# Performance work log

Hardware: AMD Instinct MI355X
Metric: run time of the kernel (lower is better)

The kernel has to match this reference:

```python
import jax, jax.numpy as jnp
import numpy as np

N_NODES, N_EDGES, B, L = 20000, 320000, 64, 48
EMB, OUT, HEADS, HID = 256, 64, 4, 512
S_DIM, R_DIM = 64, 64
TIME_NUM, CAT_NUM = 48, 201


def lrelu(x, s=0.2):
    return jnp.where(x >= 0, x, s * x)


def gru_cell(x, h, Wi, Wh, bi, bh):
    # PyTorch GRUCell math
    gi = x @ Wi.T + bi
    gh = h @ Wh.T + bh
    ir, iz, ig = jnp.split(gi, 3, axis=-1)
    hr, hz, hg = jnp.split(gh, 3, axis=-1)
    r = jax.nn.sigmoid(ir + hr)
    z = jax.nn.sigmoid(iz + hz)
    n = jnp.tanh(ig + r * hg)
    return (1.0 - z) * n + z * h


def gru_seq(x, Wi, Wh, bi, bh, reverse=False):
    # x: [B,L,D] -> [B,L,H]
    xs = jnp.swapaxes(x, 0, 1)
    if reverse:
        xs = xs[::-1]
    h0 = jnp.zeros((x.shape[0], Wh.shape[1]), x.dtype)

    def step(h, xt):
        h2 = gru_cell(xt, h, Wi, Wh, bi, bh)
        return h2, h2

    _, ys = jax.lax.scan(step, h0, xs)
    if reverse:
        ys = ys[::-1]
    return jnp.swapaxes(ys, 0, 1)


def setup_inputs() -> dict:
    key = jax.random.key(0)
    ks = iter(jax.random.split(key, 64))
    f32 = jnp.float32

    def rn(shape, s=0.1):
        return (s * jax.random.normal(next(ks), shape)).astype(f32)

    inp = {
        'graph_x': jnp.arange(N_NODES),
        'edge_index': jax.random.randint(next(ks), (2, N_EDGES), 0, N_NODES),
        'edge_attr': jax.random.uniform(next(ks), (N_EDGES,), f32),
        'batch_x': jax.random.randint(next(ks), (B, L), 0, N_NODES),
        'batch_time': jax.random.randint(next(ks), (B, L), 0, TIME_NUM),
        'batch_cat': jax.random.randint(next(ks), (B, L), 0, CAT_NUM),
        'poi_time': jax.random.randint(next(ks), (N_NODES,), 0, TIME_NUM),
        'poi_cat': jax.random.randint(next(ks), (N_NODES,), 0, CAT_NUM),
        # params
        'node_emb': rn((N_NODES, EMB), 1.0),
        'W_gat': rn((EMB, HEADS * OUT), 0.05),
        'att_src': rn((HEADS, OUT), 0.05),
        'att_dst': rn((HEADS, OUT), 0.05),
        'gat_bias': rn((HEADS * OUT,)),
        'time_table': rn((TIME_NUM, EMB), 1.0),
        'cat_table': rn((CAT_NUM, EMB), 1.0),
        'W_w': rn((EMB, 3 * EMB)), 'b_w': rn((EMB,)),
        'Wi_f': rn((3 * HID, EMB), 0.05), 'Wh_f': rn((3 * HID, HID), 0.05),
        'bi_f': jnp.zeros((3 * HID,), f32), 'bh_f': jnp.zeros((3 * HID,), f32),
        'Wi_bw': rn((3 * HID, EMB), 0.05), 'Wh_bw': rn((3 * HID, HID), 0.05),
        'bi_bw': jnp.zeros((3 * HID,), f32), 'bh_bw': jnp.zeros((3 * HID,), f32),
        'Wi_u': rn((3 * HID, 2 * HID), 0.05), 'Wh_u': rn((3 * HID, HID), 0.05),
        'bi_u': jnp.zeros((3 * HID,), f32), 'bh_u': jnp.zeros((3 * HID,), f32),
        'Ws_m': rn((S_DIM, 2 * HID)), 'bs_m': rn((S_DIM,)),
        'Ws_lv': rn((S_DIM, 2 * HID)), 'bs_lv': rn((S_DIM,)),
        'Wr_m': rn((R_DIM, HID)), 'br_m': rn((R_DIM,)),
        'Wr_lv': rn((R_DIM, HID)), 'br_lv': rn((R_DIM,)),
        'Wp1_i': rn((3 * HID, R_DIM), 0.05), 'Wp1_h': rn((3 * HID, HID), 0.05),
        'bp1_i': jnp.zeros((3 * HID,), f32), 'bp1_h': jnp.zeros((3 * HID,), f32),
        'Wp2_i': rn((3 * HID, HID), 0.05), 'Wp2_h': rn((3 * HID, HID), 0.05),
        'bp2_i': jnp.zeros((3 * HID,), f32), 'bp2_h': jnp.zeros((3 * HID,), f32),
        'Wpm': rn((R_DIM, HID)), 'bpm': rn((R_DIM,)),
        'Wplv': rn((R_DIM, HID)), 'bplv': rn((R_DIM,)),
        'Wd': rn((N_NODES, S_DIM + R_DIM)), 'bd': rn((N_NODES,)),
    }
    return inp


def forward(graph_x, edge_index, edge_attr, batch_x, batch_time, batch_cat,
            poi_time, poi_cat, node_emb, W_gat, att_src, att_dst, gat_bias,
            time_table, cat_table, W_w, b_w, Wi_f, Wh_f, bi_f, bh_f,
            Wi_bw, Wh_bw, bi_bw, bh_bw, Wi_u, Wh_u, bi_u, bh_u,
            Ws_m, bs_m, Ws_lv, bs_lv, Wr_m, br_m, Wr_lv, br_lv,
            Wp1_i, Wp1_h, bp1_i, bp1_h, Wp2_i, Wp2_h, bp2_i, bp2_h,
            Wpm, bpm, Wplv, bplv, Wd, bd):
    Bn, Ln = batch_x.shape
    N = node_emb.shape[0]
    heads, C = att_src.shape

    # --- weighted GAT layer over the POI graph ---
    h = node_emb[graph_x]                                   # [N, EMB]
    xW = (h @ W_gat).reshape(N, heads, C)                   # [N, H, C]
    src, dst = edge_index[0], edge_index[1]
    e = lrelu((xW * att_src).sum(-1)[src] + (xW * att_dst).sum(-1)[dst])  # [E, H]
    emax = jax.ops.segment_max(e, dst, num_segments=N)
    a = jnp.exp(e - emax[dst])
    asum = jax.ops.segment_sum(a, dst, num_segments=N)
    att = a / (asum[dst] + 1e-16)
    msg = (att * edge_attr[:, None])[:, :, None] * xW[src]  # [E, H, C]
    p = jax.ops.segment_sum(msg, dst, num_segments=N).reshape(N, heads * C) + gat_bias

    # --- per-step feature build ---
    p_h = p[batch_x]                                        # [B, L, EMB]
    t_e = time_table[batch_time]
    c_e = cat_table[batch_cat]
    ph = jnp.concatenate([p_h, t_e, c_e], axis=2) @ W_w.T + b_w  # [B, L, EMB]

    # --- posterior encode: biGRU -> s, uniGRU -> r ---
    f_fwd = gru_seq(ph, Wi_f, Wh_f, bi_f, bh_f)
    f_bwd = gru_seq(ph, Wi_bw, Wh_bw, bi_bw, bh_bw, reverse=True)
    features = jnp.concatenate([f_fwd, f_bwd], axis=2)      # [B, L, 2H]
    Hh = Wh_f.shape[1]
    frontal = features[:, Ln - 1, :Hh]
    backward = features[:, 0, Hh:2 * Hh]
    g = jnp.concatenate([frontal, backward], axis=1)
    s_mean = lrelu(g @ Ws_m.T + bs_m)
    s_logvar = lrelu(g @ Ws_lv.T + bs_lv)

    key = jax.random.key(42)
    k1, k2, k3 = jax.random.split(key, 3)
    s_post = s_mean + jax.random.normal(k1, s_mean.shape, s_mean.dtype) * jnp.exp(0.5 * s_logvar)

    r_feat = gru_seq(features, Wi_u, Wh_u, bi_u, bh_u)      # [B, L, H]
    r_mean = r_feat @ Wr_m.T + br_m
    r_logvar = r_feat @ Wr_lv.T + br_lv
    r_post = r_mean + jax.random.normal(k2, r_mean.shape, r_mean.dtype) * jnp.exp(0.5 * r_logvar)

    # --- prior: 2-layer GRUCell unroll fed with shifted r_post ---
    Rd = r_post.shape[2]
    r_in = jnp.concatenate([jnp.zeros((Bn, 1, Rd), r_post.dtype), r_post[:, :-1]], axis=1)
    r_in_t = jnp.swapaxes(r_in, 0, 1)                       # [L, B, R]
    eps = jax.random.normal(k3, (Ln, Bn, Rd), r_post.dtype)

    def pstep(carry, xe):
        h1, h2 = carry
        rt, ep = xe
        h1 = gru_cell(rt, h1, Wp1_i, Wp1_h, bp1_i, bp1_h)
        h2 = gru_cell(h1, h2, Wp2_i, Wp2_h, bp2_i, bp2_h)
        mt = h2 @ Wpm.T + bpm
        lvt = h2 @ Wplv.T + bplv
        rp = mt + ep * jnp.exp(0.5 * lvt)
        return (h1, h2), (mt, lvt, rp)

    h10 = jnp.zeros((Bn, Hh), r_post.dtype)
    h20 = jnp.zeros((Bn, Hh), r_post.dtype)
    _, (ms, lvs, rps) = jax.lax.scan(pstep, (h10, h20), (r_in_t, eps))
    r_mean_prior = jnp.swapaxes(ms, 0, 1)
    r_logvar_prior = jnp.swapaxes(lvs, 0, 1)
    r_prior = jnp.swapaxes(rps, 0, 1)

    # --- decode ---
    s_expand = jnp.broadcast_to(s_post[:, None, :], (Bn, Ln, s_post.shape[1]))
    zf = jnp.concatenate([r_post, s_expand], axis=2)
    recon_x = zf @ Wd.T + bd                                # [B, L, node_num]
    return (s_mean, s_logvar, s_post, r_mean, r_logvar, r_post,
            r_mean_prior, r_logvar_prior, r_prior, recon_x)


def reference(graph_x, edge_index, edge_attr, batch_x, batch_time, batch_cat,
              poi_time, poi_cat, node_emb, W_gat, att_src, att_dst, gat_bias,
              time_table, cat_table, W_w, b_w, Wi_f, Wh_f, bi_f, bh_f,
              Wi_bw, Wh_bw, bi_bw, bh_bw, Wi_u, Wh_u, bi_u, bh_u,
              Ws_m, bs_m, Ws_lv, bs_lv, Wr_m, br_m, Wr_lv, br_lv,
              Wp1_i, Wp1_h, bp1_i, bp1_h, Wp2_i, Wp2_h, bp2_i, bp2_h,
              Wpm, bpm, Wplv, bplv, Wd, bd):
    return forward(graph_x, edge_index, edge_attr, batch_x, batch_time, batch_cat,
                   poi_time, poi_cat, node_emb, W_gat, att_src, att_dst, gat_bias,
                   time_table, cat_table, W_w, b_w, Wi_f, Wh_f, bi_f, bh_f,
                   Wi_bw, Wh_bw, bi_bw, bh_bw, Wi_u, Wh_u, bi_u, bh_u,
                   Ws_m, bs_m, Ws_lv, bs_lv, Wr_m, br_m, Wr_lv, br_lv,
                   Wp1_i, Wp1_h, bp1_i, bp1_h, Wp2_i, Wp2_h, bp2_i, bp2_h,
                   Wpm, bpm, Wplv, bplv, Wd, bd)
```

## Files before the change

kernel.cpp:

```cpp
#include <hip/hip_runtime.h>
#include <stdint.h>
#include <stddef.h>

#define DEV __device__ __forceinline__

typedef float f32x4 __attribute__((ext_vector_type(4)));

__host__ __device__ inline void tf2x32(uint32_t k0, uint32_t k1,
                                       uint32_t x0, uint32_t x1,
                                       uint32_t* o0, uint32_t* o1) {
  uint32_t ks2 = k0 ^ k1 ^ 0x1BD11BDAu;
  uint32_t ks[3] = {k0, k1, ks2};
  x0 += k0; x1 += k1;
  const uint32_t R[8] = {13u,15u,26u,6u,17u,29u,16u,24u};
  for (int r = 0; r < 5; ++r) {
    const uint32_t* rot = (r & 1) ? (R + 4) : R;
    for (int i = 0; i < 4; ++i) {
      x0 += x1;
      uint32_t d = rot[i];
      x1 = (x1 << d) | (x1 >> (32u - d));
      x1 ^= x0;
    }
    x0 += ks[(r + 1) % 3];
    x1 += ks[(r + 2) % 3] + (uint32_t)(r + 1);
  }
  *o0 = x0; *o1 = x1;
}

DEV float erfinv_approx(float x) {
  float w = -logf((1.0f - x) * (1.0f + x));
  float p;
  if (w < 5.0f) {
    w = w - 2.5f;
    p = 2.81022636e-08f;
    p = fmaf(p, w, 3.43273939e-07f);
    p = fmaf(p, w, -3.5233877e-06f);
    p = fmaf(p, w, -4.39150654e-06f);
    p = fmaf(p, w, 0.00021858087f);
    p = fmaf(p, w, -0.00125372503f);
    p = fmaf(p, w, -0.00417768164f);
    p = fmaf(p, w, 0.246640727f);
    p = fmaf(p, w, 1.50140941f);
  } else {
    w = sqrtf(w) - 3.0f;
    p = -0.000200214257f;
    p = fmaf(p, w, 0.000100950558f);
    p = fmaf(p, w, 0.00134934322f);
    p = fmaf(p, w, -0.00367342844f);
    p = fmaf(p, w, 0.00573950773f);
    p = fmaf(p, w, -0.0076224613f);
    p = fmaf(p, w, 0.00943887047f);
    p = fmaf(p, w, 1.00167406f);
    p = fmaf(p, w, 2.83297682f);
  }
  return p * x;
}

DEV float normal_part(uint32_t ka, uint32_t kb, uint32_t idx) {
  uint32_t b1, b2;
  tf2x32(ka, kb, 0u, idx, &b1, &b2);
  uint32_t bits = b1 ^ b2;
  float f = __uint_as_float((bits >> 9) | 0x3f800000u) - 1.0f;
  const float lo = -0.99999994f;
  float u = f * 2.0f + lo;
  u = fmaxf(lo, u);
  return 1.41421356f * erfinv_approx(u);
}

DEV float lrelu(float x) { return x >= 0.f ? x : 0.2f * x; }
DEV float sigm(float x) { return 1.0f / (1.0f + expf(-x)); }

DEV float gru_out(float ir, float iz, float ig, float hr, float hz, float hg, float hprev) {
  float r = sigm(ir + hr);
  float z = sigm(iz + hz);
  float n = tanhf(ig + r * hg);
  return (1.0f - z) * n + z * hprev;
}

DEV float dot4f(float4 a, float4 b, float acc) {
  return fmaf(a.x, b.x, fmaf(a.y, b.y, fmaf(a.z, b.z, fmaf(a.w, b.w, acc))));
}

template <int K4>
DEV void dot2(const float* __restrict__ h, const float* __restrict__ w0,
              const float* __restrict__ w1, float& a0, float& a1) {
  const float4* h4 = (const float4*)h;
  const float4* p0 = (const float4*)w0;
  const float4* p1 = (const float4*)w1;
  #pragma unroll 4
  for (int k = 0; k < K4; ++k) {
    float4 hv = h4[k];
    float4 v0 = p0[k], v1 = p1[k];
    a0 = dot4f(hv, v0, a0);
    a1 = dot4f(hv, v1, a1);
  }
}

template <int K4>
DEV void dotT3p(const float* __restrict__ hp, int b,
                const float* __restrict__ w0, const float* __restrict__ w1,
                const float* __restrict__ w2, float& a0, float& a1, float& a2) {
  const float4* __restrict__ w04 = (const float4*)w0;
  const float4* __restrict__ w14 = (const float4*)w1;
  const float4* __restrict__ w24 = (const float4*)w2;
  const float4* __restrict__ h4 = (const float4*)hp;
  #pragma unroll
  for (int k4 = 0; k4 < K4; ++k4) {
    float4 hv = h4[k4 * 64 + b];
    a0 = dot4f(w04[k4], hv, a0);
    a1 = dot4f(w14[k4], hv, a1);
    a2 = dot4f(w24[k4], hv, a2);
  }
}

template <int K4>
DEV void dotT3_lds(const float* __restrict__ hl, int b,
                   const float* __restrict__ w0, const float* __restrict__ w1,
                   const float* __restrict__ w2, float& a0, float& a1, float& a2) {
  const float4* __restrict__ h4 = (const float4*)hl;
  const float4* __restrict__ w04 = (const float4*)w0;
  const float4* __restrict__ w14 = (const float4*)w1;
  const float4* __restrict__ w24 = (const float4*)w2;
  #pragma unroll 8
  for (int k4 = 0; k4 < K4; ++k4) {
    float4 hv = h4[k4 * 64 + b];
    a0 = dot4f(w04[k4], hv, a0);
    a1 = dot4f(w14[k4], hv, a1);
    a2 = dot4f(w24[k4], hv, a2);
  }
}

template <int N16>
DEV void stage_lds(float* __restrict__ dst, const float* __restrict__ src) {
  const float4* __restrict__ s4 = (const float4*)src;
  float4* __restrict__ d4 = (float4*)dst;
  int tid = threadIdx.x;
  constexpr int CH = (N16 < 16) ? N16 : 16;
  #pragma unroll
  for (int r = 0; r < N16; r += CH) {
    float4 v[CH];
    #pragma unroll
    for (int u = 0; u < CH; ++u) v[u] = s4[(size_t)(r + u) * 256 + tid];
    #pragma unroll
    for (int u = 0; u < CH; ++u) d4[(size_t)(r + u) * 256 + tid] = v[u];
  }
}

DEV size_t pk(int k, int b) { return (size_t)(k >> 2) * 256 + b * 4 + (k & 3); }

DEV void coh_store_i(int* p, int v) {
  asm volatile("global_store_dword %0, %1, off sc0 sc1" :: "v"(p), "v"(v) : "memory");
}
DEV void coh_store_f(float* p, float v) {
  asm volatile("global_store_dword %0, %1, off sc0 sc1" :: "v"(p), "v"(v) : "memory");
}
DEV void coh_store_f4(float* p, f32x4 v) {
  asm volatile("global_store_dwordx4 %0, %1, off sc0 sc1" :: "v"(p), "v"(v) : "memory");
}
DEV int coh_load_i(const int* p) {
  int v;
  asm volatile("global_load_dword %0, %1, off sc0 sc1\n\ts_waitcnt vmcnt(0)"
               : "=v"(v) : "v"(p) : "memory");
  return v;
}

DEV void flag_barrier(int* __restrict__ flags, int nblk, int myidx, int gen) {
  asm volatile("s_waitcnt vmcnt(0)" ::: "memory");
  __syncthreads();
  if (threadIdx.x == 0) coh_store_i(flags + myidx, gen);
  if ((int)threadIdx.x < nblk) {
    int spins = 0;
    while (coh_load_i(flags + threadIdx.x) < gen) {
      __builtin_amdgcn_s_sleep(16);
      if (++spins > (1 << 19)) break;
    }
  }
  __syncthreads();
}

DEV void wait_group(const int* __restrict__ flags, int nblk, int thr) {
  if ((int)threadIdx.x < nblk) {
    int spins = 0;
    while (coh_load_i(flags + threadIdx.x) < thr) {
      __builtin_amdgcn_s_sleep(16);
      if (++spins > (1 << 19)) break;
    }
  }
  __syncthreads();
}

DEV void store_packed_tile4(float* dst_t, const float (*smem)[64], int j0) {
  if (threadIdx.x < 64) {
    int bb = threadIdx.x;
    f32x4 v;
    v.x = smem[0][bb];
    v.y = smem[1][bb];
    v.z = smem[2][bb];
    v.w = smem[3][bb];
    coh_store_f4(dst_t + (size_t)(j0 >> 2) * 256 + bb * 4, v);
  }
}

#define GBM 128
#define GBN 128
#define GBK 16

__global__ __launch_bounds__(256) void gemm_nt(
    const float* __restrict__ A, const float* __restrict__ Bt,
    const float* __restrict__ bias, float* __restrict__ C,
    int M, int N, int K, const int* __restrict__ gatherA, int trGI) {
  __shared__ float As[GBK][GBM + 4];
  __shared__ float Bs[GBK][GBN + 4];
  const int bm = blockIdx.y * GBM;
  const int bn = blockIdx.x * GBN;
  const int tid = threadIdx.x;
  const int tx = tid & 15;
  const int ty = tid >> 4;
  float acc[8][8];
  #pragma unroll
  for (int i = 0; i < 8; ++i)
    #pragma unroll
    for (int j = 0; j < 8; ++j) acc[i][j] = 0.f;

  for (int k0 = 0; k0 < K; k0 += GBK) {
    #pragma unroll
    for (int s = 0; s < 2; ++s) {
      int f = tid + s * 256;
      int r = f >> 2, kq = f & 3;
      int row = bm + r;
      float4 v = make_float4(0.f, 0.f, 0.f, 0.f);
      if (row < M) {
        int ar = gatherA ? gatherA[row] : row;
        v = *(const float4*)&A[(size_t)ar * K + k0 + kq * 4];
      }
      As[kq * 4 + 0][r] = v.x;
      As[kq * 4 + 1][r] = v.y;
      As[kq * 4 + 2][r] = v.z;
      As[kq * 4 + 3][r] = v.w;
    }
    #pragma unroll
    for (int s = 0; s < 2; ++s) {
      int f = tid + s * 256;
      int r = f >> 2, kq = f & 3;
      int col = bn + r;
      float4 v = make_float4(0.f, 0.f, 0.f, 0.f);
      if (col < N) v = *(const float4*)&Bt[(size_t)col * K + k0 + kq * 4];
      Bs[kq * 4 + 0][r] = v.x;
      Bs[kq * 4 + 1][r] = v.y;
      Bs[kq * 4 + 2][r] = v.z;
      Bs[kq * 4 + 3][r] = v.w;
    }
    __syncthreads();
    #pragma unroll
    for (int kk = 0; kk < GBK; ++kk) {
      float4 a0 = *(const float4*)&As[kk][ty * 4];
      float4 a1 = *(const float4*)&As[kk][64 + ty * 4];
      float4 b0 = *(const float4*)&Bs[kk][tx * 4];
      float4 b1 = *(const float4*)&Bs[kk][64 + tx * 4];
      float av[8] = {a0.x, a0.y, a0.z, a0.w, a1.x, a1.y, a1.z, a1.w};
      float bv[8] = {b0.x, b0.y, b0.z, b0.w, b1.x, b1.y, b1.z, b1.w};
      #pragma unroll
      for (int i = 0; i < 8; ++i)
        #pragma unroll
        for (int j = 0; j < 8; ++j)
          acc[i][j] = fmaf(av[i], bv[j], acc[i][j]);
    }
    __syncthreads();
  }
  #pragma unroll
  for (int i = 0; i < 8; ++i) {
    int row = bm + ((i < 4) ? (ty * 4 + i) : (64 + ty * 4 + i - 4));
    if (row >= M) continue;
    if (trGI) {
      #pragma unroll
      for (int j = 0; j < 8; ++j) {
        int col = bn + ((j < 4) ? (tx * 4 + j) : (64 + tx * 4 + j - 4));
        if (col >= N) continue;
        float v = acc[i][j] + (bias ? bias[col] : 0.f);
        int bb = row / 48, tt = row - bb * 48;
        C[((size_t)tt * N + col) * 64 + bb] = v;
      }
    } else {
      #pragma unroll
      for (int g = 0; g < 2; ++g) {
        int col0 = bn + g * 64 + tx * 4;
        if (col0 + 3 >= N) continue;
        float4 v;
        v.x = acc[i][g * 4 + 0] + (bias ? bias[col0 + 0] : 0.f);
        v.y = acc[i][g * 4 + 1] + (bias ? bias[col0 + 1] : 0.f);
        v.z = acc[i][g * 4 + 2] + (bias ? bias[col0 + 2] : 0.f);
        v.w = acc[i][g * 4 + 3] + (bias ? bias[col0 + 3] : 0.f);
        *(float4*)&C[(size_t)row * N + col0] = v;
      }
    }
  }
}

__global__ void k_transpose(const float* __restrict__ W, float* __restrict__ Wt,
                            int rows, int cols) {
  int idx = blockIdx.x * 256 + threadIdx.x;
  if (idx >= rows * cols) return;
  int r = idx / cols, c = idx % cols;
  Wt[(size_t)c * rows + r] = W[idx];
}

__global__ void k_count_deg(const int* __restrict__ dst, int* __restrict__ deg, int nE) {
  int e = blockIdx.x * 256 + threadIdx.x;
  if (e < nE) atomicAdd(&deg[dst[e]], 1);
}

__global__ __launch_bounds__(1024) void k_scan(const int* __restrict__ deg,
                                               int* __restrict__ off,
                                               int* __restrict__ cursor, int n) {
  __shared__ int tmp[1024];
  __shared__ int carry_s;
  if (threadIdx.x == 0) carry_s = 0;
  __syncthreads();
  for (int base = 0; base < n; base += 1024) {
    int i = base + (int)threadIdx.x;
    int v = (i < n) ? deg[i] : 0;
    tmp[threadIdx.x] = v;
    __syncthreads();
    for (int s = 1; s < 1024; s <<= 1) {
      int t = (threadIdx.x >= (unsigned)s) ? tmp[threadIdx.x - s] : 0;
      __syncthreads();
      tmp[threadIdx.x] += t;
      __syncthreads();
    }
    int incl = tmp[threadIdx.x];
    int base_c = carry_s;
    int excl = incl - v;
    if (i < n) { off[i] = base_c + excl; cursor[i] = base_c + excl; }
    __syncthreads();
    if (threadIdx.x == 1023) carry_s = base_c + incl;
    __syncthreads();
  }
  if (threadIdx.x == 0) off[n] = carry_s;
}

__global__ void k_scatter(const int* __restrict__ dst, int* __restrict__ cursor,
                          int* __restrict__ csr, int nE) {
  int e = blockIdx.x * 256 + threadIdx.x;
  if (e < nE) {
    int pos = atomicAdd(&cursor[dst[e]], 1);
    csr[pos] = e;
  }
}

__global__ void k_alpha(const float* __restrict__ xW, const float* __restrict__ att_src,
                        const float* __restrict__ att_dst, float* __restrict__ as_,
                        float* __restrict__ ad_) {
  int i = blockIdx.x * 256 + threadIdx.x;
  if (i >= 80000) return;
  int n = i >> 2, h = i & 3;
  const float* xr = xW + (size_t)n * 256 + h * 64;
  const float* s = att_src + h * 64;
  const float* d = att_dst + h * 64;
  float a = 0.f, b = 0.f;
  dot2<16>(xr, s, d, a, b);
  as_[i] = a;
  ad_[i] = b;
}

__global__ __launch_bounds__(256) void k_gat_node(
    const float* __restrict__ xW, const float* __restrict__ as_,
    const float* __restrict__ ad_, const int* __restrict__ off,
    const int* __restrict__ csr, const int* __restrict__ esrc,
    const float* __restrict__ eattr, const float* __restrict__ gat_bias,
    float* __restrict__ p) {
  int n = blockIdx.x;
  int h = threadIdx.x >> 6;
  int c = threadIdx.x & 63;
  int s0 = off[n], s1 = off[n + 1];
  float adn = ad_[n * 4 + h];
  float m = -3.0e38f;
  for (int idx = s0; idx < s1; ++idx) {
    int e = csr[idx];
    int s = esrc[e];
    float ev = lrelu(as_[s * 4 + h] + adn);
    m = fmaxf(m, ev);
  }
  float sum = 0.f;
  for (int idx = s0; idx < s1; ++idx) {
    int e = csr[idx];
    int s = esrc[e];
    float ev = lrelu(as_[s * 4 + h] + adn);
    sum += expf(ev - m);
  }
  float acc = 0.f;
  for (int idx = s0; idx < s1; ++idx) {
    int e = csr[idx];
    int s = esrc[e];
    float ev = lrelu(as_[s * 4 + h] + adn);
    float w = expf(ev - m) / (sum + 1e-16f) * eattr[e];
    acc = fmaf(w, xW[(size_t)s * 256 + h * 64 + c], acc);
  }
  p[(size_t)n * 256 + h * 64 + c] = acc + gat_bias[h * 64 + c];
}

__global__ void k_build_X(const float* __restrict__ p, const float* __restrict__ tt,
                          const float* __restrict__ ct, const int* __restrict__ bx,
                          const int* __restrict__ btm, const int* __restrict__ bct,
                          float* __restrict__ X) {
  int idx = blockIdx.x * 256 + threadIdx.x;
  if (idx >= 3072 * 768) return;
  int rl = idx / 768, c = idx % 768;
  float v;
  if (c < 256) v = p[(size_t)bx[rl] * 256 + c];
  else if (c < 512) v = tt[(size_t)btm[rl] * 256 + (c - 256)];
  else v = ct[(size_t)bct[rl] * 256 + (c - 512)];
  X[idx] = v;
}

__global__ __launch_bounds__(256, 1) void k_gru_bidir_fused(
    const float* __restrict__ giT_f, const float* __restrict__ giT_b,
    const float* __restrict__ Wh_f, const float* __restrict__ bh_f,
    const float* __restrict__ Wh_b, const float* __restrict__ bh_b,
    float* __restrict__ features, float* __restrict__ hTb,
    int* __restrict__ flags) {
  __shared__ float lds_h[32768];
  __shared__ float smem[4][64];
  int w = threadIdx.x >> 6;
  int b = threadIdx.x & 63;
  int slot = blockIdx.x * 4 + w;
  int dir = slot >> 9;
  int j = slot & 511;
  int j0 = (blockIdx.x * 4) & 511;
  int gbid = blockIdx.x & 127;
  int* gflags = flags + dir * 128;
  const float* Wh = dir ? Wh_b : Wh_f;
  const float* bh = dir ? bh_b : bh_f;
  const float* gi = dir ? giT_b : giT_f;
  const float* w0 = Wh + (size_t)j * 512;
  const float* w1 = Wh + (size_t)(512 + j) * 512;
  const float* w2 = Wh + (size_t)(1024 + j) * 512;
  float bhr = bh[j], bhz = bh[512 + j], bhg = bh[1024 + j];
  float* hD = hTb + (size_t)dir * 48 * 32768;
  for (int s = 0; s < 48; ++s) {
    int t = dir ? (47 - s) : s;
    const float* gir = gi + (size_t)t * 98304;
    float giv0 = gir[j * 64 + b];
    float giv1 = gir[(512 + j) * 64 + b];
    float giv2 = gir[(1024 + j) * 64 + b];
    float hr = bhr, hz = bhz, hg = bhg, hprev = 0.f;
    if (s > 0) {
      int tp = dir ? (t + 1) : (t - 1);
      stage_lds<32>(lds_h, hD + (size_t)tp * 32768);
      __syncthreads();
      dotT3_lds<128>(lds_h, b, w0, w1, w2, hr, hz, hg);
      hprev = lds_h[pk(j, b)];
    }
    float hnew = gru_out(giv0, giv1, giv2, hr, hz, hg, hprev);
    smem[w][b] = hnew;
    features[((size_t)(b * 48 + t)) * 1024 + dir * 512 + j] = hnew;
    __syncthreads();
    store_packed_tile4(hD + (size_t)t * 32768, smem, j0);
    flag_barrier(gflags, 128, gbid, s + 1);
  }
}

__global__ __launch_bounds__(256, 1) void k_gru_u_fused(
    const float* __restrict__ giT, const float* __restrict__ Wh,
    const float* __restrict__ bh, float* __restrict__ r_feat,
    float* __restrict__ hU, int* __restrict__ flags) {
  __shared__ float lds_h[32768];
  __shared__ float smem[4][64];
  int w = threadIdx.x >> 6;
  int b = threadIdx.x & 63;
  int j = blockIdx.x * 4 + w;
  int j0 = blockIdx.x * 4;
  const float* w0 = Wh + (size_t)j * 512;
  const float* w1 = Wh + (size_t)(512 + j) * 512;
  const float* w2 = Wh + (size_t)(1024 + j) * 512;
  float bhr = bh[j], bhz = bh[512 + j], bhg = bh[1024 + j];
  for (int s = 0; s < 48; ++s) {
    const float* gir = giT + (size_t)s * 98304;
    float giv0 = gir[j * 64 + b];
    float giv1 = gir[(512 + j) * 64 + b];
    float giv2 = gir[(1024 + j) * 64 + b];
    float hr = bhr, hz = bhz, hg = bhg, hprev = 0.f;
    if (s > 0) {
      stage_lds<32>(lds_h, hU + (size_t)(s - 1) * 32768);
      __syncthreads();
      dotT3_lds<128>(lds_h, b, w0, w1, w2, hr, hz, hg);
      hprev = lds_h[pk(j, b)];
    }
    float hnew = gru_out(giv0, giv1, giv2, hr, hz, hg, hprev);
    smem[w][b] = hnew;
    r_feat[((size_t)(b * 48 + s)) * 512 + j] = hnew;
    __syncthreads();
    store_packed_tile4(hU + (size_t)s * 32768, smem, j0);
    flag_barrier(flags, 128, blockIdx.x, s + 1);
  }
}

__global__ __launch_bounds__(256, 1) void k_prior_fused(
    const float* __restrict__ r_post,
    const float* __restrict__ Wp1_i, const float* __restrict__ Wp1_h,
    const float* __restrict__ bp1_i, const float* __restrict__ bp1_h,
    const float* __restrict__ Wp2_i, const float* __restrict__ Wp2_h,
    const float* __restrict__ bp2_i, const float* __restrict__ bp2_h,
    float* __restrict__ h1S, float* __restrict__ h2S,
    float* __restrict__ rT, int* __restrict__ flags) {
  __shared__ float lds_h[32768];
  __shared__ float smem[4][64];
  int w = threadIdx.x >> 6;
  int b = threadIdx.x & 63;
  int cell = blockIdx.x >> 7;
  int gbid = blockIdx.x & 127;
  int slot = blockIdx.x * 4 + w;
  int j = slot & 511;
  int j0 = (blockIdx.x * 4) & 511;
  int* flagsA = flags;
  int* flagsB = flags + 128;

  if (cell == 0) {
    int tid = gbid * 256 + threadIdx.x;
    for (int x = tid; x < 48 * 64 * 64; x += 32768) {
      int b0 = x & 63;
      int i0 = (x >> 6) & 63;
      int t0 = x >> 12;
      coh_store_f(rT + (size_t)t0 * 4096 + pk(i0, b0),
                  r_post[((size_t)(b0 * 48 + t0)) * 64 + i0]);
    }
    flag_barrier(flagsA, 128, gbid, 1);

    const float* wi0 = Wp1_i + (size_t)j * 64;
    const float* wi1 = Wp1_i + (size_t)(512 + j) * 64;
    const float* wi2 = Wp1_i + (size_t)(1024 + j) * 64;
    const float* wh0 = Wp1_h + (size_t)j * 512;
    const float* wh1 = Wp1_h + (size_t)(512 + j) * 512;
    const float* wh2 = Wp1_h + (size_t)(1024 + j) * 512;
    float bir = bp1_i[j], biz = bp1_i[512 + j], big = bp1_i[1024 + j];
    float bhr = bp1_h[j], bhz = bp1_h[512 + j], bhg = bp1_h[1024 + j];
    for (int k = 0; k < 48; ++k) {
      float ir = bir, iz = biz, ig = big;
      float hr = bhr, hz = bhz, hg = bhg, hprev = 0.f;
      if (k > 0) {
        stage_lds<32>(lds_h, h1S + (size_t)(k - 1) * 32768);
        dotT3p<16>(rT + (size_t)(k - 1) * 4096, b, wi0, wi1, wi2, ir, iz, ig);
        __syncthreads();
        dotT3_lds<128>(lds_h, b, wh0, wh1, wh2, hr, hz, hg);
        hprev = lds_h[pk(j, b)];
      }
      smem[w][b] = gru_out(ir, iz, ig, hr, hz, hg, hprev);
      __syncthreads();
      store_packed_tile4(h1S + (size_t)k * 32768, smem, j0);
      flag_barrier(flagsA, 128, gbid, k + 2);
    }
  } else {
    const float* wi0 = Wp2_i + (size_t)j * 512;
    const float* wi1 = Wp2_i + (size_t)(512 + j) * 512;
    const float* wi2 = Wp2_i + (size_t)(1024 + j) * 512;
    const float* wh0 = Wp2_h + (size_t)j * 512;
    const float* wh1 = Wp2_h + (size_t)(512 + j) * 512;
    const float* wh2 = Wp2_h + (size_t)(1024 + j) * 512;
    float bir = bp2_i[j], biz = bp2_i[512 + j], big = bp2_i[1024 + j];
    float bhr = bp2_h[j], bhz = bp2_h[512 + j], bhg = bp2_h[1024 + j];
    for (int t = 0; t < 48; ++t) {
      wait_group(flagsA, 128, t + 2);
      stage_lds<32>(lds_h, h1S + (size_t)t * 32768);
      __syncthreads();
      float ir = bir, iz = biz, ig = big;
      dotT3_lds<128>(lds_h, b, wi0, wi1, wi2, ir, iz, ig);
      float hr = bhr, hz = bhz, hg = bhg, hprev = 0.f;
      if (t > 0) {
        __syncthreads();
        stage_lds<32>(lds_h, h2S + (size_t)(t - 1) * 32768);
        __syncthreads();
        dotT3_lds<128>(lds_h, b, wh0, wh1, wh2, hr, hz, hg);
        hprev = lds_h[pk(j, b)];
      }
      smem[w][b] = gru_out(ir, iz, ig, hr, hz, hg, hprev);
      __syncthreads();
      store_packed_tile4(h2S + (size_t)t * 32768, smem, j0);
      flag_barrier(flagsB, 128, gbid, t + 1);
    }
  }
}

__global__ void k_s_head(const float* __restrict__ features,
                         const float* __restrict__ Ws_m, const float* __restrict__ bs_m,
                         const float* __restrict__ Ws_lv, const float* __restrict__ bs_lv,
                         float* __restrict__ out, uint32_t ka, uint32_t kb) {
  int idx = blockIdx.x * 256 + threadIdx.x;
  if (idx >= 4096) return;
  int i = idx & 63, b = idx >> 6;
  const float* fr = features + ((size_t)(b * 48 + 47)) * 1024;
  const float* bk = features + ((size_t)(b * 48 + 0)) * 1024 + 512;
  const float* wm = Ws_m + (size_t)i * 1024;
  const float* wl = Ws_lv + (size_t)i * 1024;
  float m = 0.f, lv = 0.f;
  dot2<128>(fr, wm, wl, m, lv);
  dot2<128>(bk, wm + 512, wl + 512, m, lv);
  m = lrelu(m + bs_m[i]);
  lv = lrelu(lv + bs_lv[i]);
  float nz = normal_part(ka, kb, (uint32_t)idx);
  out[idx] = m;
  out[4096 + idx] = lv;
  out[8192 + idx] = m + nz * expf(0.5f * lv);
}

__global__ void k_r_head(const float* __restrict__ r_feat,
                         const float* __restrict__ Wr_m, const float* __restrict__ br_m,
                         const float* __restrict__ Wr_lv, const float* __restrict__ br_lv,
                         float* __restrict__ out, uint32_t ka, uint32_t kb) {
  int idx = blockIdx.x * 256 + threadIdx.x;
  if (idx >= 196608) return;
  int i = idx & 63;
  int bt = idx >> 6;
  const float* f = r_feat + (size_t)bt * 512;
  float m = 0.f, lv = 0.f;
  dot2<128>(f, Wr_m + (size_t)i * 512, Wr_lv + (size_t)i * 512, m, lv);
  m += br_m[i];
  lv += br_lv[i];
  float nz = normal_part(ka, kb, (uint32_t)idx);
  out[12288 + idx] = m;
  out[208896 + idx] = lv;
  out[405504 + idx] = m + nz * expf(0.5f * lv);
}

__global__ void k_prior_out(const float* __restrict__ h2S,
                            const float* __restrict__ Wpm, const float* __restrict__ bpm,
                            const float* __restrict__ Wplv, const float* __restrict__ bplv,
                            float* __restrict__ out, uint32_t ka, uint32_t kb) {
  int idx = blockIdx.x * 256 + threadIdx.x;
  if (idx >= 196608) return;
  int i = idx & 63;
  int bt = idx >> 6;
  int b = bt & 63;
  int t = bt >> 6;
  const float4* h4 = (const float4*)(h2S + (size_t)t * 32768);
  const float4* wm4 = (const float4*)(Wpm + (size_t)i * 512);
  const float4* wl4 = (const float4*)(Wplv + (size_t)i * 512);
  float m = 0.f, lv = 0.f;
  #pragma unroll 8
  for (int k4 = 0; k4 < 128; ++k4) {
    float4 hv = h4[k4 * 64 + b];
    m = dot4f(wm4[k4], hv, m);
    lv = dot4f(wl4[k4], hv, lv);
  }
  m += bpm[i];
  lv += bplv[i];
  float ep = normal_part(ka, kb, (uint32_t)idx);
  float rp = m + ep * expf(0.5f * lv);
  size_t o = ((size_t)b * 48 + t) * 64 + i;
  out[602112 + o] = m;
  out[798720 + o] = lv;
  out[995328 + o] = rp;
}

__global__ void k_build_zf(const float* __restrict__ out, float* __restrict__ zf) {
  int idx = blockIdx.x * 256 + threadIdx.x;
  if (idx >= 3072 * 128) return;
  int row = idx >> 7, c = idx & 127;
  float v;
  if (c < 64) v = out[405504 + row * 64 + c];
  else v = out[8192 + (row / 48) * 64 + (c - 64)];
  zf[idx] = v;
}

extern "C" void kernel_launch(void* const* d_in, const int* in_sizes, int n_in,
                              void* d_out, int out_size, void* d_ws, size_t ws_size,
                              hipStream_t stream) {
  const int* graph_x = (const int*)d_in[0];
  const int* edge_index = (const int*)d_in[1];
  const float* edge_attr = (const float*)d_in[2];
  const int* batch_x = (const int*)d_in[3];
  const int* batch_time = (const int*)d_in[4];
  const int* batch_cat = (const int*)d_in[5];
  const float* node_emb = (const float*)d_in[8];
  const float* W_gat = (const float*)d_in[9];
  const float* att_src = (const float*)d_in[10];
  const float* att_dst = (const float*)d_in[11];
  const float* gat_bias = (const float*)d_in[12];
  const float* time_table = (const float*)d_in[13];
  const float* cat_table = (const float*)d_in[14];
  const float* W_w = (const float*)d_in[15];
  const float* b_w = (const float*)d_in[16];
  const float* Wi_f = (const float*)d_in[17];
  const float* Wh_f = (const float*)d_in[18];
  const float* bi_f = (const float*)d_in[19];
  const float* bh_f = (const float*)d_in[20];
  const float* Wi_bw = (const float*)d_in[21];
  const float* Wh_bw = (const float*)d_in[22];
  const float* bi_bw = (const float*)d_in[23];
  const float* bh_bw = (const float*)d_in[24];
  const float* Wi_u = (const float*)d_in[25];
  const float* Wh_u = (const float*)d_in[26];
  const float* bi_u = (const float*)d_in[27];
  const float* bh_u = (const float*)d_in[28];
  const float* Ws_m = (const float*)d_in[29];
  const float* bs_m = (const float*)d_in[30];
  const float* Ws_lv = (const float*)d_in[31];
  const float* bs_lv = (const float*)d_in[32];
  const float* Wr_m = (const float*)d_in[33];
  const float* br_m = (const float*)d_in[34];
  const float* Wr_lv = (const float*)d_in[35];
  const float* br_lv = (const float*)d_in[36];
  const float* Wp1_i = (const float*)d_in[37];
  const float* Wp1_h = (const float*)d_in[38];
  const float* bp1_i = (const float*)d_in[39];
  const float* bp1_h = (const float*)d_in[40];
  const float* Wp2_i = (const float*)d_in[41];
  const float* Wp2_h = (const float*)d_in[42];
  const float* bp2_i = (const float*)d_in[43];
  const float* bp2_h = (const float*)d_in[44];
  const float* Wpm = (const float*)d_in[45];
  const float* bpm = (const float*)d_in[46];
  const float* Wplv = (const float*)d_in[47];
  const float* bplv = (const float*)d_in[48];
  const float* Wd = (const float*)d_in[49];
  const float* bd = (const float*)d_in[50];
  float* out = (float*)d_out;

  uint32_t k1a, k1b, k2a, k2b, k3a, k3b;
  tf2x32(0u, 42u, 0u, 0u, &k1a, &k1b);
  tf2x32(0u, 42u, 0u, 1u, &k2a, &k2b);
  tf2x32(0u, 42u, 0u, 2u, &k3a, &k3b);

  float* ws = (float*)d_ws;
  size_t o = 0;
  auto alloc = [&](size_t n) { float* q = ws + o; o += n; return q; };
  float* R1 = alloc(5120000);
  float* R2 = alloc(5120000);
  float* R3 = alloc(4718592);
  float* R4 = alloc(786432);
  float* as_ = alloc(80000);
  float* ad_ = alloc(80000);
  float* Wgt = alloc(65536);
  int* deg = (int*)alloc(20000);
  int* off = (int*)alloc(20001);
  int* cursor = (int*)alloc(20000);
  int* csr = (int*)alloc(320000);
  float* rT = alloc(196608);
  int* flags = (int*)alloc(1024);

  float* xW = R1;
  float* features = R1;
  float* r_feat = R1 + 3145728;
  float* p = R2;
  float* giT_b = R2;
  float* hU = R2;
  float* X = R3;
  float* giT_f = R3;
  float* giT_u = R3;
  float* h1S = R3;
  float* h2S = R3 + 1572864;
  float* ph = R4;
  float* zf = R4;
  float* hTb = out + 1191936;

  const int* esrc = edge_index;
  const int* edst = edge_index + 320000;

  dim3 B(256);

  (void)hipMemsetAsync(deg, 0, 20000 * sizeof(int), stream);
  (void)hipMemsetAsync(flags, 0, 1024 * sizeof(int), stream);

  k_transpose<<<dim3(256), B, 0, stream>>>(W_gat, Wgt, 256, 256);
  k_count_deg<<<dim3(1250), B, 0, stream>>>(edst, deg, 320000);
  k_scan<<<dim3(1), dim3(1024), 0, stream>>>(deg, off, cursor, 20000);
  k_scatter<<<dim3(1250), B, 0, stream>>>(edst, cursor, csr, 320000);
  gemm_nt<<<dim3(2, 157), B, 0, stream>>>(node_emb, Wgt, nullptr, xW,
                                          20000, 256, 256, graph_x, 0);
  k_alpha<<<dim3(313), B, 0, stream>>>(xW, att_src, att_dst, as_, ad_);
  k_gat_node<<<dim3(20000), B, 0, stream>>>(xW, as_, ad_, off, csr, esrc,
                                            edge_attr, gat_bias, p);

  k_build_X<<<dim3(9216), B, 0, stream>>>(p, time_table, cat_table, batch_x,
                                          batch_time, batch_cat, X);
  gemm_nt<<<dim3(2, 24), B, 0, stream>>>(X, W_w, b_w, ph, 3072, 256, 768,
                                         nullptr, 0);

  gemm_nt<<<dim3(12, 24), B, 0, stream>>>(ph, Wi_f, bi_f, giT_f, 3072, 1536, 256,
                                          nullptr, 1);
  gemm_nt<<<dim3(12, 24), B, 0, stream>>>(ph, Wi_bw, bi_bw, giT_b, 3072, 1536, 256,
                                          nullptr, 1);
  k_gru_bidir_fused<<<dim3(256), B, 0, stream>>>(
      giT_f, giT_b, Wh_f, bh_f, Wh_bw, bh_bw, features, hTb, flags);

  k_s_head<<<dim3(16), B, 0, stream>>>(features, Ws_m, bs_m, Ws_lv, bs_lv,
                                       out, k1a, k1b);

  gemm_nt<<<dim3(12, 24), B, 0, stream>>>(features, Wi_u, bi_u, giT_u,
                                          3072, 1536, 1024, nullptr, 1);
  k_gru_u_fused<<<dim3(128), B, 0, stream>>>(giT_u, Wh_u, bh_u, r_feat,
                                             hU, flags + 256);

  k_r_head<<<dim3(768), B, 0, stream>>>(r_feat, Wr_m, br_m, Wr_lv, br_lv,
                                        out, k2a, k2b);

  k_prior_fused<<<dim3(256), B, 0, stream>>>(
      out + 405504, Wp1_i, Wp1_h, bp1_i, bp1_h, Wp2_i, Wp2_h, bp2_i, bp2_h,
      h1S, h2S, rT, flags + 384);
  k_prior_out<<<dim3(768), B, 0, stream>>>(h2S, Wpm, bpm, Wplv, bplv,
                                           out, k3a, k3b);

  k_build_zf<<<dim3(1536), B, 0, stream>>>(out, zf);
  gemm_nt<<<dim3(157, 24), B, 0, stream>>>(zf, Wd, bd, out + 1191936,
                                           3072, 20000, 128, nullptr, 0);
}
```

Measured before the change: 5.106 ms.

## Use 1024-thread blocks in persistent GRU kernels to cut grid barrier participants

The persistent recurrent GRU kernels (bidirectional, u, prior) now run 16 hidden units per block with 1024 threads instead of 4 units with 256 threads. The grid shrinks by 4x, so each per-step flag barrier waits on 32 blocks rather than 128, and each block stages the previous hidden state into LDS once for four times as many output units. Staging and packed-store helpers were rewritten for the wider blocks. In exchange, only 32-64 CUs are used, which lowers aggregate bandwidth for the weight reads done every step.

```diff
diff --git a/kernel.cpp b/kernel.cpp
--- a/kernel.cpp
+++ b/kernel.cpp
@@ -130,20 +130,15 @@
   }
 }
 
-template <int N16>
-DEV void stage_lds(float* __restrict__ dst, const float* __restrict__ src) {
+DEV void stage_lds1k(float* __restrict__ dst, const float* __restrict__ src) {
   const float4* __restrict__ s4 = (const float4*)src;
   float4* __restrict__ d4 = (float4*)dst;
   int tid = threadIdx.x;
-  constexpr int CH = (N16 < 16) ? N16 : 16;
+  float4 v[8];
   #pragma unroll
-  for (int r = 0; r < N16; r += CH) {
-    float4 v[CH];
-    #pragma unroll
-    for (int u = 0; u < CH; ++u) v[u] = s4[(size_t)(r + u) * 256 + tid];
-    #pragma unroll
-    for (int u = 0; u < CH; ++u) d4[(size_t)(r + u) * 256 + tid] = v[u];
-  }
+  for (int u = 0; u < 8; ++u) v[u] = s4[(size_t)u * 1024 + tid];
+  #pragma unroll
+  for (int u = 0; u < 8; ++u) d4[(size_t)u * 1024 + tid] = v[u];
 }
 
 DEV size_t pk(int k, int b) { return (size_t)(k >> 2) * 256 + b * 4 + (k & 3); }
@@ -189,15 +184,16 @@
   __syncthreads();
 }
 
-DEV void store_packed_tile4(float* dst_t, const float (*smem)[64], int j0) {
-  if (threadIdx.x < 64) {
-    int bb = threadIdx.x;
+DEV void store_packed_tile16(float* dst_t, const float (*smem)[64], int j0) {
+  if (threadIdx.x < 256) {
+    int q = threadIdx.x >> 6;
+    int bb = threadIdx.x & 63;
     f32x4 v;
-    v.x = smem[0][bb];
-    v.y = smem[1][bb];
-    v.z = smem[2][bb];
-    v.w = smem[3][bb];
-    coh_store_f4(dst_t + (size_t)(j0 >> 2) * 256 + bb * 4, v);
+    v.x = smem[q * 4 + 0][bb];
+    v.y = smem[q * 4 + 1][bb];
+    v.z = smem[q * 4 + 2][bb];
+    v.w = smem[q * 4 + 3][bb];
+    coh_store_f4(dst_t + (size_t)((j0 >> 2) + q) * 256 + bb * 4, v);
   }
 }
 
@@ -412,21 +408,21 @@
   X[idx] = v;
 }
 
-__global__ __launch_bounds__(256, 1) void k_gru_bidir_fused(
+
+__global__ __launch_bounds__(1024, 1) void k_gru_bidir_fused(
     const float* __restrict__ giT_f, const float* __restrict__ giT_b,
     const float* __restrict__ Wh_f, const float* __restrict__ bh_f,
     const float* __restrict__ Wh_b, const float* __restrict__ bh_b,
     float* __restrict__ features, float* __restrict__ hTb,
     int* __restrict__ flags) {
   __shared__ float lds_h[32768];
-  __shared__ float smem[4][64];
+  __shared__ float smem[16][64];
   int w = threadIdx.x >> 6;
   int b = threadIdx.x & 63;
-  int slot = blockIdx.x * 4 + w;
-  int dir = slot >> 9;
-  int j = slot & 511;
-  int j0 = (blockIdx.x * 4) & 511;
-  int gbid = blockIdx.x & 127;
+  int dir = blockIdx.x >> 5;
+  int gbid = blockIdx.x & 31;
+  int j0 = gbid * 16;
+  int j = j0 + w;
   int* gflags = flags + dir * 128;
   const float* Wh = dir ? Wh_b : Wh_f;
   const float* bh = dir ? bh_b : bh_f;
@@ -445,7 +441,7 @@
     float hr = bhr, hz = bhz, hg = bhg, hprev = 0.f;
     if (s > 0) {
       int tp = dir ? (t + 1) : (t - 1);
-      stage_lds<32>(lds_h, hD + (size_t)tp * 32768);
+      stage_lds1k(lds_h, hD + (size_t)tp * 32768);
       __syncthreads();
       dotT3_lds<128>(lds_h, b, w0, w1, w2, hr, hz, hg);
       hprev = lds_h[pk(j, b)];
@@ -454,21 +450,21 @@
     smem[w][b] = hnew;
     features[((size_t)(b * 48 + t)) * 1024 + dir * 512 + j] = hnew;
     __syncthreads();
-    store_packed_tile4(hD + (size_t)t * 32768, smem, j0);
-    flag_barrier(gflags, 128, gbid, s + 1);
-  }
-}
-
-__global__ __launch_bounds__(256, 1) void k_gru_u_fused(
+    store_packed_tile16(hD + (size_t)t * 32768, smem, j0);
+    flag_barrier(gflags, 32, gbid, s + 1);
+  }
+}
+
+__global__ __launch_bounds__(1024, 1) void k_gru_u_fused(
     const float* __restrict__ giT, const float* __restrict__ Wh,
     const float* __restrict__ bh, float* __restrict__ r_feat,
     float* __restrict__ hU, int* __restrict__ flags) {
   __shared__ float lds_h[32768];
-  __shared__ float smem[4][64];
+  __shared__ float smem[16][64];
   int w = threadIdx.x >> 6;
   int b = threadIdx.x & 63;
-  int j = blockIdx.x * 4 + w;
-  int j0 = blockIdx.x * 4;
+  int j0 = blockIdx.x * 16;
+  int j = j0 + w;
   const float* w0 = Wh + (size_t)j * 512;
   const float* w1 = Wh + (size_t)(512 + j) * 512;
   const float* w2 = Wh + (size_t)(1024 + j) * 512;
@@ -480,7 +476,7 @@
     float giv2 = gir[(1024 + j) * 64 + b];
     float hr = bhr, hz = bhz, hg = bhg, hprev = 0.f;
     if (s > 0) {
-      stage_lds<32>(lds_h, hU + (size_t)(s - 1) * 32768);
+      stage_lds1k(lds_h, hU + (size_t)(s - 1) * 32768);
       __syncthreads();
       dotT3_lds<128>(lds_h, b, w0, w1, w2, hr, hz, hg);
       hprev = lds_h[pk(j, b)];
@@ -489,12 +485,12 @@
     smem[w][b] = hnew;
     r_feat[((size_t)(b * 48 + s)) * 512 + j] = hnew;
     __syncthreads();
-    store_packed_tile4(hU + (size_t)s * 32768, smem, j0);
-    flag_barrier(flags, 128, blockIdx.x, s + 1);
-  }
-}
-
-__global__ __launch_bounds__(256, 1) void k_prior_fused(
+    store_packed_tile16(hU + (size_t)s * 32768, smem, j0);
+    flag_barrier(flags, 32, blockIdx.x, s + 1);
+  }
+}
+
+__global__ __launch_bounds__(1024, 1) void k_prior_fused(
     const float* __restrict__ r_post,
     const float* __restrict__ Wp1_i, const float* __restrict__ Wp1_h,
     const float* __restrict__ bp1_i, const float* __restrict__ bp1_h,
@@ -503,19 +499,18 @@
     float* __restrict__ h1S, float* __restrict__ h2S,
     float* __restrict__ rT, int* __restrict__ flags) {
   __shared__ float lds_h[32768];
-  __shared__ float smem[4][64];
+  __shared__ float smem[16][64];
   int w = threadIdx.x >> 6;
   int b = threadIdx.x & 63;
-  int cell = blockIdx.x >> 7;
-  int gbid = blockIdx.x & 127;
-  int slot = blockIdx.x * 4 + w;
-  int j = slot & 511;
-  int j0 = (blockIdx.x * 4) & 511;
+  int cell = blockIdx.x >> 5;
+  int gbid = blockIdx.x & 31;
+  int j0 = gbid * 16;
+  int j = j0 + w;
   int* flagsA = flags;
   int* flagsB = flags + 128;
 
   if (cell == 0) {
-    int tid = gbid * 256 + threadIdx.x;
+    int tid = gbid * 1024 + threadIdx.x;
     for (int x = tid; x < 48 * 64 * 64; x += 32768) {
       int b0 = x & 63;
       int i0 = (x >> 6) & 63;
@@ -523,7 +518,7 @@
       coh_store_f(rT + (size_t)t0 * 4096 + pk(i0, b0),
                   r_post[((size_t)(b0 * 48 + t0)) * 64 + i0]);
     }
-    flag_barrier(flagsA, 128, gbid, 1);
+    flag_barrier(flagsA, 32, gbid, 1);
 
     const float* wi0 = Wp1_i + (size_t)j * 64;
     const float* wi1 = Wp1_i + (size_t)(512 + j) * 64;
@@ -537,7 +532,7 @@
       float ir = bir, iz = biz, ig = big;
       float hr = bhr, hz = bhz, hg = bhg, hprev = 0.f;
       if (k > 0) {
-        stage_lds<32>(lds_h, h1S + (size_t)(k - 1) * 32768);
+        stage_lds1k(lds_h, h1S + (size_t)(k - 1) * 32768);
         dotT3p<16>(rT + (size_t)(k - 1) * 4096, b, wi0, wi1, wi2, ir, iz, ig);
         __syncthreads();
         dotT3_lds<128>(lds_h, b, wh0, wh1, wh2, hr, hz, hg);
@@ -545,8 +540,8 @@
       }
       smem[w][b] = gru_out(ir, iz, ig, hr, hz, hg, hprev);
       __syncthreads();
-      store_packed_tile4(h1S + (size_t)k * 32768, smem, j0);
-      flag_barrier(flagsA, 128, gbid, k + 2);
+      store_packed_tile16(h1S + (size_t)k * 32768, smem, j0);
+      flag_barrier(flagsA, 32, gbid, k + 2);
     }
   } else {
     const float* wi0 = Wp2_i + (size_t)j * 512;
@@ -558,23 +553,23 @@
     float bir = bp2_i[j], biz = bp2_i[512 + j], big = bp2_i[1024 + j];
     float bhr = bp2_h[j], bhz = bp2_h[512 + j], bhg = bp2_h[1024 + j];
     for (int t = 0; t < 48; ++t) {
-      wait_group(flagsA, 128, t + 2);
-      stage_lds<32>(lds_h, h1S + (size_t)t * 32768);
+      wait_group(flagsA, 32, t + 2);
+      stage_lds1k(lds_h, h1S + (size_t)t * 32768);
       __syncthreads();
       float ir = bir, iz = biz, ig = big;
       dotT3_lds<128>(lds_h, b, wi0, wi1, wi2, ir, iz, ig);
       float hr = bhr, hz = bhz, hg = bhg, hprev = 0.f;
       if (t > 0) {
         __syncthreads();
-        stage_lds<32>(lds_h, h2S + (size_t)(t - 1) * 32768);
+        stage_lds1k(lds_h, h2S + (size_t)(t - 1) * 32768);
         __syncthreads();
         dotT3_lds<128>(lds_h, b, wh0, wh1, wh2, hr, hz, hg);
         hprev = lds_h[pk(j, b)];
       }
       smem[w][b] = gru_out(ir, iz, ig, hr, hz, hg, hprev);
       __syncthreads();
-      store_packed_tile4(h2S + (size_t)t * 32768, smem, j0);
-      flag_barrier(flagsB, 128, gbid, t + 1);
+      store_packed_tile16(h2S + (size_t)t * 32768, smem, j0);
+      flag_barrier(flagsB, 32, gbid, t + 1);
     }
   }
 }
@@ -778,7 +773,7 @@
                                           nullptr, 1);
   gemm_nt<<<dim3(12, 24), B, 0, stream>>>(ph, Wi_bw, bi_bw, giT_b, 3072, 1536, 256,
                                           nullptr, 1);
-  k_gru_bidir_fused<<<dim3(256), B, 0, stream>>>(
+  k_gru_bidir_fused<<<dim3(64), dim3(1024), 0, stream>>>(
       giT_f, giT_b, Wh_f, bh_f, Wh_bw, bh_bw, features, hTb, flags);
 
   k_s_head<<<dim3(16), B, 0, stream>>>(features, Ws_m, bs_m, Ws_lv, bs_lv,
@@ -786,13 +781,13 @@
 
   gemm_nt<<<dim3(12, 24), B, 0, stream>>>(features, Wi_u, bi_u, giT_u,
                                           3072, 1536, 1024, nullptr, 1);
-  k_gru_u_fused<<<dim3(128), B, 0, stream>>>(giT_u, Wh_u, bh_u, r_feat,
-                                             hU, flags + 256);
+  k_gru_u_fused<<<dim3(32), dim3(1024), 0, stream>>>(giT_u, Wh_u, bh_u, r_feat,
+                                                     hU, flags + 256);
 
   k_r_head<<<dim3(768), B, 0, stream>>>(r_feat, Wr_m, br_m, Wr_lv, br_lv,
                                         out, k2a, k2b);
 
-  k_prior_fused<<<dim3(256), B, 0, stream>>>(
+  k_prior_fused<<<dim3(64), dim3(1024), 0, stream>>>(
       out + 405504, Wp1_i, Wp1_h, bp1_i, bp1_h, Wp2_i, Wp2_h, bp2_i, bp2_h,
       h1S, h2S, rT, flags + 384);
   k_prior_out<<<dim3(768), B, 0, stream>>>(h2S, Wpm, bpm, Wplv, bplv,
```

After: 10.34 ms. 2.03x slower.
